# Kernel tuning notes

Measured on AMD Instinct MI355X. Metric: run time of the kernel, lower is better.

Reference implementation:

```python
import jax, jax.numpy as jnp
import numpy as np

D_EMB_IN = 1024
D_K = 64
D_EMB_OUT = 1024
NB_HEADS = 16


def setup_inputs() -> dict:
    key = jax.random.key(0)
    k1, k2, k3, k4, k5 = jax.random.split(key, 5)
    scale = 0.02
    X = jax.random.normal(k1, (2, 2048, D_EMB_IN), dtype=jnp.float32)
    # nn.Linear weights are [out, in]; we store them transposed-ready as [in, out]
    Wq = jax.random.normal(k2, (D_EMB_IN, NB_HEADS * D_K), dtype=jnp.float32) * scale
    Wk = jax.random.normal(k3, (D_EMB_IN, NB_HEADS * D_K), dtype=jnp.float32) * scale
    Wv = jax.random.normal(k4, (D_EMB_IN, NB_HEADS * D_K), dtype=jnp.float32) * scale
    Wo = jax.random.normal(k5, (NB_HEADS * D_K, D_EMB_OUT), dtype=jnp.float32) * scale
    return {"X": X, "Wq": Wq, "Wk": Wk, "Wv": Wv, "Wo": Wo}


def reference(X, Wq, Wk, Wv, Wo):
    B, T, _ = X.shape
    H, Dk = NB_HEADS, D_K
    # project and split heads: [B, H, T, Dk]
    def proj(W):
        return (X @ W).reshape(B, T, H, Dk).transpose(0, 2, 1, 3)
    Q, K, V = proj(Wq), proj(Wk), proj(Wv)
    S = jnp.einsum("bhqd,bhkd->bhqk", Q, K) / jnp.sqrt(jnp.float32(Dk))
    causal = jnp.tril(jnp.ones((T, T), dtype=bool))  # True = keep
    S = jnp.where(causal, S, -jnp.inf)
    P = jax.nn.softmax(S, axis=-1)
    A = jnp.einsum("bhqk,bhkd->bhqd", P, V)
    A = A.transpose(0, 2, 1, 3).reshape(B, T, H * Dk)
    return A @ Wo
```

## Files before the change

### kernel.cpp

```cpp
#include <hip/hip_runtime.h>
#include <hip/hip_bf16.h>


typedef unsigned short u16;
typedef __bf16 bf16x8 __attribute__((ext_vector_type(8)));
typedef float f32x4 __attribute__((ext_vector_type(4)));
typedef u16 u16x4 __attribute__((ext_vector_type(4)));

#define TS 72
#define PS 136
#define NEG_INF (-1e30f)
#define SC_LOG2 0.1803368801f

#if __has_builtin(__builtin_amdgcn_exp2f)
#define EXP2(x) __builtin_amdgcn_exp2f(x)
#else
#define EXP2(x) exp2f(x)
#endif

#define GLD_LDS16(gp, lp) __builtin_amdgcn_global_load_lds( \
    (const __attribute__((address_space(1))) void*)(gp),    \
    (__attribute__((address_space(3))) void*)(lp), 16, 0, 0)

__device__ __forceinline__ bf16x8 as_bf16x8(int4 v) { return __builtin_bit_cast(bf16x8, v); }
__device__ __forceinline__ u16 bf16_bits(float f) { return __builtin_bit_cast(u16, (__bf16)f); }

__device__ __forceinline__ bool detect_f32(const void* X) {
    const u16* x16 = (const u16*)X;
    int lane = threadIdx.x & 63;
    int hits = 0;
#pragma unroll
    for (int i = 0; i < 4; ++i) {
        u16 v = x16[lane * 4 + i];
        hits += (((v >> 7) & 0xFF) > 130) ? 1 : 0;
    }
    return __popcll(__ballot(hits > 0)) >= 8;
}

__device__ __forceinline__ bf16x8 load8(const void* p, size_t eoff, bool f32m) {
    if (!f32m) return as_bf16x8(*(const int4*)((const u16*)p + eoff));
    const float* f = (const float*)p + eoff;
    float4 a = *(const float4*)f;
    float4 b = *(const float4*)(f + 4);
    bf16x8 r;
    r[0] = (__bf16)a.x; r[1] = (__bf16)a.y; r[2] = (__bf16)a.z; r[3] = (__bf16)a.w;
    r[4] = (__bf16)b.x; r[5] = (__bf16)b.y; r[6] = (__bf16)b.z; r[7] = (__bf16)b.w;
    return r;
}

__global__ __launch_bounds__(256) void prep_all(const void* __restrict__ Wq,
                                                const void* __restrict__ Wk,
                                                const void* __restrict__ Wv,
                                                const void* __restrict__ Wo,
                                                const void* __restrict__ X,
                                                u16* __restrict__ Wt3,
                                                u16* __restrict__ Wot,
                                                u16* __restrict__ Xbf) {
    bool f32m = detect_f32(X);
    int z = blockIdx.z;
    if (z == 4) {
        int blk = blockIdx.y * 16 + blockIdx.x;
        size_t base = (size_t)blk * 16384 + threadIdx.x * 8;
#pragma unroll
        for (int i = 0; i < 8; ++i) {
            size_t eoff = base + (size_t)i * 2048;
            bf16x8 v = load8(X, eoff, f32m);
            *(int4*)(Xbf + eoff) = __builtin_bit_cast(int4, v);
        }
        return;
    }
    const void* in = (z == 0) ? Wq : (z == 1) ? Wk : (z == 2) ? Wv : Wo;
    u16* out = (z < 3) ? (Wt3 + (size_t)z * (1u << 20)) : Wot;
    __shared__ alignas(16) u16 T[64][TS];
    int r0 = blockIdx.y * 64, c0 = blockIdx.x * 64;
    int tr = threadIdx.x >> 3, tc8 = threadIdx.x & 7;
    bf16x8 v0 = load8(in, (size_t)(r0 + tr) * 1024 + c0 + tc8 * 8, f32m);
    bf16x8 v1 = load8(in, (size_t)(r0 + tr + 32) * 1024 + c0 + tc8 * 8, f32m);
    *(int4*)&T[tr][tc8 * 8]      = __builtin_bit_cast(int4, v0);
    *(int4*)&T[tr + 32][tc8 * 8] = __builtin_bit_cast(int4, v1);
    __syncthreads();
    for (int half = 0; half < 2; ++half) {
        int cr = tr + half * 32;
        u16 tmp[8];
#pragma unroll
        for (int i = 0; i < 8; ++i) tmp[i] = T[tc8 * 8 + i][cr];
        *(int4*)(out + (size_t)(c0 + cr) * 1024 + r0 + tc8 * 8) = *(int4*)tmp;
    }
}

__global__ __launch_bounds__(256, 4) void gemm128(const u16* __restrict__ A,
                                                  const u16* __restrict__ Bt,
                                                  u16* __restrict__ Cq, u16* __restrict__ Ck,
                                                  u16* __restrict__ Cv) {
    __shared__ alignas(16) u16 As[128 * 64];
    __shared__ alignas(16) u16 Bs[128 * 64];
    const int K = 1024;
    int tid = threadIdx.x, wave = tid >> 6, lane = tid & 63;
    int quad = lane >> 4, l16 = lane & 15;
    int wrow = wave >> 1, wcol = wave & 1;
    int m0 = blockIdx.x * 128, n0 = blockIdx.y * 128;
    int rlane = lane >> 3, kc = lane & 7;
    int scol = (kc ^ rlane) * 8;

    f32x4 acc[4][4] = {};

    for (int k0 = 0; k0 < K; k0 += 64) {
        __syncthreads();
#pragma unroll
        for (int i = 0; i < 4; ++i) {
            int rc = wave * 4 + i;
            GLD_LDS16(A  + (size_t)(m0 + rc * 8 + rlane) * K + k0 + scol, As + rc * 512);
            GLD_LDS16(Bt + (size_t)(n0 + rc * 8 + rlane) * K + k0 + scol, Bs + rc * 512);
        }
        __syncthreads();
#pragma unroll
        for (int ks = 0; ks < 2; ++ks) {
            bf16x8 af[4], bfr[4];
#pragma unroll
            for (int i = 0; i < 4; ++i) {
                int row = wrow * 64 + i * 16 + l16;
                af[i] = as_bf16x8(*(const int4*)(As + row * 64 + (((ks * 4 + quad) ^ (row & 7)) * 8)));
            }
#pragma unroll
            for (int j = 0; j < 4; ++j) {
                int row = wcol * 64 + j * 16 + l16;
                bfr[j] = as_bf16x8(*(const int4*)(Bs + row * 64 + (((ks * 4 + quad) ^ (row & 7)) * 8)));
            }
#pragma unroll
            for (int i = 0; i < 4; ++i)
#pragma unroll
                for (int j = 0; j < 4; ++j)
                    acc[i][j] = __builtin_amdgcn_mfma_f32_16x16x32_bf16(af[i], bfr[j], acc[i][j], 0, 0, 0);
        }
    }

#pragma unroll
    for (int i = 0; i < 4; ++i)
#pragma unroll
        for (int j = 0; j < 4; ++j)
#pragma unroll
            for (int r = 0; r < 4; ++r) {
                int m = m0 + wrow * 64 + i * 16 + quad * 4 + r;
                int n = n0 + wcol * 64 + j * 16 + l16;
                float f = acc[i][j][r];
                if (n < 1024)       Cq[(size_t)m * 1024 + n] = bf16_bits(f);
                else if (n < 2048)  Ck[(size_t)m * 1024 + n - 1024] = bf16_bits(f);
                else {
                    int n2 = n - 2048;
                    int bh = ((m >> 11) << 4) | (n2 >> 6), d = n2 & 63, t = m & 2047;
                    Cv[(((size_t)bh * 64 + d) << 11) + t] = bf16_bits(f);
                }
            }
}

__global__ __launch_bounds__(256, 4) void gemm_out(const u16* __restrict__ A,
                                                   const u16* __restrict__ Bt,
                                                   void* __restrict__ Cout,
                                                   const void* __restrict__ Xdet) {
    bool f32m = detect_f32(Xdet);
    __shared__ alignas(16) u16 As[64 * 128];
    __shared__ alignas(16) u16 Bs[128 * 128];
    const int K = 1024;
    int tid = threadIdx.x, wave = tid >> 6, lane = tid & 63;
    int quad = lane >> 4, l16 = lane & 15;
    int wrow = wave & 1, wcol = wave >> 1;
    int m0 = blockIdx.x * 64, n0 = blockIdx.y * 128;
    int rlane4 = lane >> 4, kc16 = lane & 15;

    f32x4 acc[2][4] = {};

    for (int k0 = 0; k0 < K; k0 += 128) {
        __syncthreads();
#pragma unroll
        for (int i = 0; i < 8; ++i) {
            int rb = wave * 32 + i * 4;
            int grow = rb + rlane4;
            int gch = kc16 ^ (grow & 15);
            GLD_LDS16(Bt + (size_t)(n0 + grow) * K + k0 + gch * 8, Bs + rb * 128);
        }
#pragma unroll
        for (int i = 0; i < 4; ++i) {
            int rb = wave * 16 + i * 4;
            int grow = rb + rlane4;
            int gch = kc16 ^ (grow & 15);
            GLD_LDS16(A + (size_t)(m0 + grow) * K + k0 + gch * 8, As + rb * 128);
        }
        __syncthreads();
#pragma unroll
        for (int ks = 0; ks < 4; ++ks) {
            bf16x8 af[2], bfr[4];
#pragma unroll
            for (int i = 0; i < 2; ++i) {
                int row = wrow * 32 + i * 16 + l16;
                af[i] = as_bf16x8(*(const int4*)(As + row * 128 + (((ks * 4 + quad) ^ (row & 15)) * 8)));
            }
#pragma unroll
            for (int j = 0; j < 4; ++j) {
                int row = wcol * 64 + j * 16 + l16;
                bfr[j] = as_bf16x8(*(const int4*)(Bs + row * 128 + (((ks * 4 + quad) ^ (row & 15)) * 8)));
            }
#pragma unroll
            for (int i = 0; i < 2; ++i)
#pragma unroll
                for (int j = 0; j < 4; ++j)
                    acc[i][j] = __builtin_amdgcn_mfma_f32_16x16x32_bf16(af[i], bfr[j], acc[i][j], 0, 0, 0);
        }
    }

#pragma unroll
    for (int i = 0; i < 2; ++i)
#pragma unroll
        for (int j = 0; j < 4; ++j)
#pragma unroll
            for (int r = 0; r < 4; ++r) {
                int m = m0 + wrow * 32 + i * 16 + quad * 4 + r;
                int n = n0 + wcol * 64 + j * 16 + l16;
                float f = acc[i][j][r];
                if (f32m) ((float*)Cout)[(size_t)m * 1024 + n] = f;
                else      ((u16*)Cout)[(size_t)m * 1024 + n] = bf16_bits(f);
            }
}

__global__ __launch_bounds__(512, 4) void attn_kernel(const u16* __restrict__ Qb,
                                                      const u16* __restrict__ Kb,
                                                      const u16* __restrict__ Vt,
                                                      u16* __restrict__ Ab) {
    __shared__ alignas(16) u16 Ks[128 * 64];
    __shared__ alignas(16) u16 Vs[64 * 128];
    __shared__ alignas(16) u16 Ps[128 * PS];

    int tid = threadIdx.x, wave = tid >> 6, lane = tid & 63;
    int quad = lane >> 4, l16 = lane & 15;
    int bh = blockIdx.x;
    int J = (blockIdx.y < 8) ? (15 - (int)blockIdx.y) : ((int)blockIdx.y - 8);
    int b = bh >> 4, h = bh & 15;
    int q0 = J * 128;
    int kr4 = lane >> 3, kc = lane & 7;
    int vr4 = lane >> 4, vc = lane & 15;

    const u16* qrow = Qb + (size_t)(b * 2048 + q0 + wave * 16 + l16) * 1024 + h * 64;
    bf16x8 qa0 = as_bf16x8(*(const int4*)(qrow + quad * 8));
    bf16x8 qa1 = as_bf16x8(*(const int4*)(qrow + 32 + quad * 8));

    f32x4 o[4] = {};
    float psum = 0.0f;

    const u16* kbase = Kb + (size_t)(b * 2048) * 1024 + h * 64;
    const u16* vbase = Vt + (size_t)bh * 64 * 2048;

    for (int j2 = 0; j2 <= J; ++j2) {
        int t0 = j2 * 128;
        __syncthreads();
#pragma unroll
        for (int i = 0; i < 2; ++i) {
            int rb = (wave * 2 + i) * 8;
            int grow = rb + kr4;
            int gch = kc ^ (grow & 7);
            GLD_LDS16(kbase + (size_t)(t0 + grow) * 1024 + gch * 8, Ks + rb * 64);
        }
#pragma unroll
        for (int i = 0; i < 2; ++i) {
            int rb = (wave * 2 + i) * 4;
            int grow = rb + vr4;
            int gch = vc ^ (grow & 15);
            GLD_LDS16(vbase + (size_t)grow * 2048 + t0 + gch * 8, Vs + rb * 128);
        }
        __syncthreads();

        bool diag = (j2 == J);
        int ntc = diag ? ((wave & ~1) + 2) : 8;

        f32x4 s[8];
        __builtin_amdgcn_s_setprio(1);
#pragma unroll
        for (int nt = 0; nt < 8; ++nt) {
            if (nt >= ntc) continue;
            if (diag && nt > wave) {
                s[nt][0] = NEG_INF; s[nt][1] = NEG_INF; s[nt][2] = NEG_INF; s[nt][3] = NEG_INF;
                continue;
            }
            int row = nt * 16 + l16;
            int sw = row & 7;
            f32x4 a = {};
            bf16x8 b0 = as_bf16x8(*(const int4*)(Ks + row * 64 + ((quad ^ sw) * 8)));
            a = __builtin_amdgcn_mfma_f32_16x16x32_bf16(b0, qa0, a, 0, 0, 0);
            bf16x8 b1 = as_bf16x8(*(const int4*)(Ks + row * 64 + (((4 + quad) ^ sw) * 8)));
            a = __builtin_amdgcn_mfma_f32_16x16x32_bf16(b1, qa1, a, 0, 0, 0);
            a = a * SC_LOG2;
            if (diag && nt == wave) {
#pragma unroll
                for (int r = 0; r < 4; ++r)
                    if (quad * 4 + r > l16) a[r] = NEG_INF;
            }
            s[nt] = a;
        }
        __builtin_amdgcn_s_setprio(0);

        int prow = (wave * 16 + l16) * PS;
#pragma unroll
        for (int nt = 0; nt < 8; ++nt) {
            if (nt >= ntc) continue;
            u16x4 pk;
            float ps4 = 0.0f;
#pragma unroll
            for (int r = 0; r < 4; ++r) {
                float p = EXP2(s[nt][r]);
                ps4 += p;
                pk[r] = bf16_bits(p);
            }
            psum += ps4;
            *(u16x4*)(Ps + prow + nt * 16 + quad * 4) = pk;
        }

        int ksm = ntc >> 1;
        __builtin_amdgcn_s_setprio(1);
#pragma unroll
        for (int ks = 0; ks < 4; ++ks) {
            if (ks >= ksm) continue;
            bf16x8 pa = as_bf16x8(*(const int4*)(Ps + (wave * 16 + l16) * PS + ks * 32 + quad * 8));
#pragma unroll
            for (int d4 = 0; d4 < 4; ++d4) {
                int vrow = d4 * 16 + l16;
                bf16x8 vb = as_bf16x8(*(const int4*)(Vs + vrow * 128 + (((ks * 4 + quad) ^ l16) * 8)));
                o[d4] = __builtin_amdgcn_mfma_f32_16x16x32_bf16(pa, vb, o[d4], 0, 0, 0);
            }
        }
        __builtin_amdgcn_s_setprio(0);
    }

    psum += __shfl_xor(psum, 16);
    psum += __shfl_xor(psum, 32);

    u16* arow = Ab + (size_t)(b * 2048 + q0 + wave * 16) * 1024 + h * 64;
#pragma unroll
    for (int r = 0; r < 4; ++r) {
        float dn = __shfl(psum, quad * 4 + r, 16);
        float inv = 1.0f / dn;
#pragma unroll
        for (int d4 = 0; d4 < 4; ++d4)
            arow[(quad * 4 + r) * 1024 + d4 * 16 + l16] = bf16_bits(o[d4][r] * inv);
    }
}

extern "C" void kernel_launch(void* const* d_in, const int* in_sizes, int n_in,
                              void* d_out, int out_size, void* d_ws, size_t ws_size,
                              hipStream_t stream) {
    (void)in_sizes; (void)n_in; (void)out_size; (void)ws_size;
    const void* X  = d_in[0];
    const void* Wq = d_in[1];
    const void* Wk = d_in[2];
    const void* Wv = d_in[3];
    const void* Wo = d_in[4];
    u16* ws16 = (u16*)d_ws;
    const size_t M1 = 1u << 20;
    u16* Xbf = ws16 + 0 * M1;
    u16* Wt3 = ws16 + 4 * M1;
    u16* Qb  = ws16 + 7 * M1;
    u16* Kb  = ws16 + 11 * M1;
    u16* Vt  = ws16 + 15 * M1;
    u16* Wot = ws16 + 19 * M1;
    u16* Ab  = ws16 + 0 * M1;

    prep_all<<<dim3(16, 16, 5), 256, 0, stream>>>(Wq, Wk, Wv, Wo, X, Wt3, Wot, Xbf);
    gemm128<<<dim3(32, 24), 256, 0, stream>>>(Xbf, Wt3, Qb, Kb, Vt);
    attn_kernel<<<dim3(32, 16), 512, 0, stream>>>(Qb, Kb, Vt, Ab);
    gemm_out<<<dim3(64, 8), 256, 0, stream>>>(Ab, Wot, d_out, X);
}
```

Before: 168.3 us.

## Prefetch next K/V tile into registers to overlap global loads with compute

```diff
diff --git a/kernel.cpp b/kernel.cpp
--- a/kernel.cpp
+++ b/kernel.cpp
@@ -248,25 +248,33 @@
     const u16* kbase = Kb + (size_t)(b * 2048) * 1024 + h * 64;
     const u16* vbase = Vt + (size_t)bh * 64 * 2048;
 
+    int rbk0 = (wave * 2 + 0) * 8, rbk1 = (wave * 2 + 1) * 8;
+    int rbv0 = (wave * 2 + 0) * 4, rbv1 = (wave * 2 + 1) * 4;
+    const u16* kgp0 = kbase + (size_t)(rbk0 + kr4) * 1024 + (kc ^ ((rbk0 + kr4) & 7)) * 8;
+    const u16* kgp1 = kbase + (size_t)(rbk1 + kr4) * 1024 + (kc ^ ((rbk1 + kr4) & 7)) * 8;
+    const u16* vgp0 = vbase + (size_t)(rbv0 + vr4) * 2048 + (vc ^ ((rbv0 + vr4) & 15)) * 8;
+    const u16* vgp1 = vbase + (size_t)(rbv1 + vr4) * 2048 + (vc ^ ((rbv1 + vr4) & 15)) * 8;
+    u16* klp0 = Ks + rbk0 * 64 + lane * 8;
+    u16* klp1 = Ks + rbk1 * 64 + lane * 8;
+    u16* vlp0 = Vs + rbv0 * 128 + lane * 8;
+    u16* vlp1 = Vs + rbv1 * 128 + lane * 8;
+
+    int4 kr0, kr1, vv0, vv1;
+    kr0 = *(const int4*)(kgp0);
+    kr1 = *(const int4*)(kgp1);
+    vv0 = *(const int4*)(vgp0);
+    vv1 = *(const int4*)(vgp1);
+    *(int4*)klp0 = kr0; *(int4*)klp1 = kr1;
+    *(int4*)vlp0 = vv0; *(int4*)vlp1 = vv1;
+    if (J >= 1) {
+        kr0 = *(const int4*)(kgp0 + (size_t)128 * 1024);
+        kr1 = *(const int4*)(kgp1 + (size_t)128 * 1024);
+        vv0 = *(const int4*)(vgp0 + 128);
+        vv1 = *(const int4*)(vgp1 + 128);
+    }
+    __syncthreads();
+
     for (int j2 = 0; j2 <= J; ++j2) {
-        int t0 = j2 * 128;
-        __syncthreads();
-#pragma unroll
-        for (int i = 0; i < 2; ++i) {
-            int rb = (wave * 2 + i) * 8;
-            int grow = rb + kr4;
-            int gch = kc ^ (grow & 7);
-            GLD_LDS16(kbase + (size_t)(t0 + grow) * 1024 + gch * 8, Ks + rb * 64);
-        }
-#pragma unroll
-        for (int i = 0; i < 2; ++i) {
-            int rb = (wave * 2 + i) * 4;
-            int grow = rb + vr4;
-            int gch = vc ^ (grow & 15);
-            GLD_LDS16(vbase + (size_t)grow * 2048 + t0 + gch * 8, Vs + rb * 128);
-        }
-        __syncthreads();
-
         bool diag = (j2 == J);
         int ntc = diag ? ((wave & ~1) + 2) : 8;
 
@@ -326,6 +334,20 @@
             }
         }
         __builtin_amdgcn_s_setprio(0);
+
+        if (j2 < J) {
+            __syncthreads();
+            *(int4*)klp0 = kr0; *(int4*)klp1 = kr1;
+            *(int4*)vlp0 = vv0; *(int4*)vlp1 = vv1;
+            if (j2 + 2 <= J) {
+                size_t t0n = (size_t)(j2 + 2) * 128;
+                kr0 = *(const int4*)(kgp0 + t0n * 1024);
+                kr1 = *(const int4*)(kgp1 + t0n * 1024);
+                vv0 = *(const int4*)(vgp0 + t0n);
+                vv1 = *(const int4*)(vgp1 + t0n);
+            }
+            __syncthreads();
+        }
     }
 
     psum += __shfl_xor(psum, 16);
```

Measured after the change: 179.1 us. +6.4%, slower.

## Double-buffer K/V tiles in attention and interleave softmax with PV per chunk

Applied to the files above, without the earlier changes.

```diff
diff --git a/kernel.cpp b/kernel.cpp
--- a/kernel.cpp
+++ b/kernel.cpp
@@ -8,7 +8,7 @@
 typedef u16 u16x4 __attribute__((ext_vector_type(4)));
 
 #define TS 72
-#define PS 136
+#define PSQ 40
 #define NEG_INF (-1e30f)
 #define SC_LOG2 0.1803368801f
 
@@ -221,13 +221,95 @@
             }
 }
 
+
+#define STAGE_TILE(KSBUF, VSBUF, T0)                                           \
+    {                                                                          \
+        _Pragma("unroll")                                                      \
+        for (int i_ = 0; i_ < 2; ++i_) {                                       \
+            int rb_ = (wave * 2 + i_) * 8;                                     \
+            int grow_ = rb_ + kr4;                                             \
+            int gch_ = kc ^ (grow_ & 7);                                       \
+            GLD_LDS16(kbase + (size_t)((T0) + grow_) * 1024 + gch_ * 8,        \
+                      KSBUF + rb_ * 64);                                       \
+        }                                                                      \
+        _Pragma("unroll")                                                      \
+        for (int i_ = 0; i_ < 2; ++i_) {                                       \
+            int rb_ = (wave * 2 + i_) * 4;                                     \
+            int grow_ = rb_ + vr4;                                             \
+            int gch_ = vc ^ (grow_ & 15);                                      \
+            GLD_LDS16(vbase + (size_t)grow_ * 2048 + (T0) + gch_ * 8,          \
+                      VSBUF + rb_ * 128);                                      \
+        }                                                                      \
+    }
+
+#define COMPUTE_TILE(KS, VS, DIAG, NTC)                                        \
+    {                                                                          \
+        _Pragma("unroll")                                                      \
+        for (int g = 0; g < 4; ++g) {                                          \
+            if (2 * g >= (NTC)) continue;                                      \
+            f32x4 sg0, sg1;                                                    \
+            __builtin_amdgcn_s_setprio(1);                                     \
+            _Pragma("unroll")                                                  \
+            for (int h2 = 0; h2 < 2; ++h2) {                                   \
+                int nt = 2 * g + h2;                                           \
+                f32x4 a = {};                                                  \
+                if ((DIAG) && nt > wave) {                                     \
+                    a[0] = NEG_INF; a[1] = NEG_INF;                            \
+                    a[2] = NEG_INF; a[3] = NEG_INF;                            \
+                } else {                                                       \
+                    int row = nt * 16 + l16;                                   \
+                    int sw = row & 7;                                          \
+                    bf16x8 b0 = as_bf16x8(*(const int4*)((KS) + row * 64 + ((quad ^ sw) * 8)));       \
+                    a = __builtin_amdgcn_mfma_f32_16x16x32_bf16(b0, qa0, a, 0, 0, 0);                 \
+                    bf16x8 b1 = as_bf16x8(*(const int4*)((KS) + row * 64 + (((4 + quad) ^ sw) * 8))); \
+                    a = __builtin_amdgcn_mfma_f32_16x16x32_bf16(b1, qa1, a, 0, 0, 0);                 \
+                    a = a * SC_LOG2;                                           \
+                    if ((DIAG) && nt == wave) {                                \
+                        _Pragma("unroll")                                      \
+                        for (int r = 0; r < 4; ++r)                            \
+                            if (quad * 4 + r > l16) a[r] = NEG_INF;            \
+                    }                                                          \
+                }                                                              \
+                if (h2 == 0) sg0 = a; else sg1 = a;                            \
+            }                                                                  \
+            __builtin_amdgcn_s_setprio(0);                                     \
+            _Pragma("unroll")                                                  \
+            for (int h2 = 0; h2 < 2; ++h2) {                                   \
+                f32x4 sv = h2 ? sg1 : sg0;                                     \
+                u16x4 pk;                                                      \
+                float ps4 = 0.0f;                                              \
+                _Pragma("unroll")                                              \
+                for (int r = 0; r < 4; ++r) {                                  \
+                    float p = EXP2(sv[r]);                                     \
+                    ps4 += p;                                                  \
+                    pk[r] = bf16_bits(p);                                      \
+                }                                                              \
+                psum += ps4;                                                   \
+                *(u16x4*)(Ps + prow + h2 * 16 + quad * 4) = pk;                \
+            }                                                                  \
+            __builtin_amdgcn_s_setprio(1);                                     \
+            {                                                                  \
+                bf16x8 pa = as_bf16x8(*(const int4*)(Ps + prow + quad * 8));   \
+                _Pragma("unroll")                                              \
+                for (int d4 = 0; d4 < 4; ++d4) {                               \
+                    int vrow = d4 * 16 + l16;                                  \
+                    bf16x8 vb = as_bf16x8(*(const int4*)((VS) + vrow * 128 + (((g * 4 + quad) ^ l16) * 8))); \
+                    o[d4] = __builtin_amdgcn_mfma_f32_16x16x32_bf16(pa, vb, o[d4], 0, 0, 0);          \
+                }                                                              \
+            }                                                                  \
+            __builtin_amdgcn_s_setprio(0);                                     \
+        }                                                                      \
+    }
+
 __global__ __launch_bounds__(512, 4) void attn_kernel(const u16* __restrict__ Qb,
                                                       const u16* __restrict__ Kb,
                                                       const u16* __restrict__ Vt,
                                                       u16* __restrict__ Ab) {
-    __shared__ alignas(16) u16 Ks[128 * 64];
-    __shared__ alignas(16) u16 Vs[64 * 128];
-    __shared__ alignas(16) u16 Ps[128 * PS];
+    __shared__ alignas(16) u16 Ks0[128 * 64];
+    __shared__ alignas(16) u16 Ks1[128 * 64];
+    __shared__ alignas(16) u16 Vs0[64 * 128];
+    __shared__ alignas(16) u16 Vs1[64 * 128];
+    __shared__ alignas(16) u16 Ps[128 * PSQ];
 
     int tid = threadIdx.x, wave = tid >> 6, lane = tid & 63;
     int quad = lane >> 4, l16 = lane & 15;
@@ -244,88 +326,30 @@
 
     f32x4 o[4] = {};
     float psum = 0.0f;
+    int prow = (wave * 16 + l16) * PSQ;
 
     const u16* kbase = Kb + (size_t)(b * 2048) * 1024 + h * 64;
     const u16* vbase = Vt + (size_t)bh * 64 * 2048;
 
-    for (int j2 = 0; j2 <= J; ++j2) {
-        int t0 = j2 * 128;
-        __syncthreads();
-#pragma unroll
-        for (int i = 0; i < 2; ++i) {
-            int rb = (wave * 2 + i) * 8;
-            int grow = rb + kr4;
-            int gch = kc ^ (grow & 7);
-            GLD_LDS16(kbase + (size_t)(t0 + grow) * 1024 + gch * 8, Ks + rb * 64);
-        }
-#pragma unroll
-        for (int i = 0; i < 2; ++i) {
-            int rb = (wave * 2 + i) * 4;
-            int grow = rb + vr4;
-            int gch = vc ^ (grow & 15);
-            GLD_LDS16(vbase + (size_t)grow * 2048 + t0 + gch * 8, Vs + rb * 128);
-        }
-        __syncthreads();
-
-        bool diag = (j2 == J);
-        int ntc = diag ? ((wave & ~1) + 2) : 8;
-
-        f32x4 s[8];
-        __builtin_amdgcn_s_setprio(1);
-#pragma unroll
-        for (int nt = 0; nt < 8; ++nt) {
-            if (nt >= ntc) continue;
-            if (diag && nt > wave) {
-                s[nt][0] = NEG_INF; s[nt][1] = NEG_INF; s[nt][2] = NEG_INF; s[nt][3] = NEG_INF;
-                continue;
-            }
-            int row = nt * 16 + l16;
-            int sw = row & 7;
-            f32x4 a = {};
-            bf16x8 b0 = as_bf16x8(*(const int4*)(Ks + row * 64 + ((quad ^ sw) * 8)));
-            a = __builtin_amdgcn_mfma_f32_16x16x32_bf16(b0, qa0, a, 0, 0, 0);
-            bf16x8 b1 = as_bf16x8(*(const int4*)(Ks + row * 64 + (((4 + quad) ^ sw) * 8)));
-            a = __builtin_amdgcn_mfma_f32_16x16x32_bf16(b1, qa1, a, 0, 0, 0);
-            a = a * SC_LOG2;
-            if (diag && nt == wave) {
-#pragma unroll
-                for (int r = 0; r < 4; ++r)
-                    if (quad * 4 + r > l16) a[r] = NEG_INF;
-            }
-            s[nt] = a;
-        }
-        __builtin_amdgcn_s_setprio(0);
-
-        int prow = (wave * 16 + l16) * PS;
-#pragma unroll
-        for (int nt = 0; nt < 8; ++nt) {
-            if (nt >= ntc) continue;
-            u16x4 pk;
-            float ps4 = 0.0f;
-#pragma unroll
-            for (int r = 0; r < 4; ++r) {
-                float p = EXP2(s[nt][r]);
-                ps4 += p;
-                pk[r] = bf16_bits(p);
-            }
-            psum += ps4;
-            *(u16x4*)(Ps + prow + nt * 16 + quad * 4) = pk;
-        }
-
-        int ksm = ntc >> 1;
-        __builtin_amdgcn_s_setprio(1);
-#pragma unroll
-        for (int ks = 0; ks < 4; ++ks) {
-            if (ks >= ksm) continue;
-            bf16x8 pa = as_bf16x8(*(const int4*)(Ps + (wave * 16 + l16) * PS + ks * 32 + quad * 8));
-#pragma unroll
-            for (int d4 = 0; d4 < 4; ++d4) {
-                int vrow = d4 * 16 + l16;
-                bf16x8 vb = as_bf16x8(*(const int4*)(Vs + vrow * 128 + (((ks * 4 + quad) ^ l16) * 8)));
-                o[d4] = __builtin_amdgcn_mfma_f32_16x16x32_bf16(pa, vb, o[d4], 0, 0, 0);
-            }
-        }
-        __builtin_amdgcn_s_setprio(0);
+    STAGE_TILE(Ks0, Vs0, 0);
+    __syncthreads();
+
+    for (int j2 = 0; j2 <= J; j2 += 2) {
+        if (j2 + 1 <= J) STAGE_TILE(Ks1, Vs1, (j2 + 1) * 128);
+        {
+            bool diag = (j2 == J);
+            int ntc = diag ? ((wave & ~1) + 2) : 8;
+            COMPUTE_TILE(Ks0, Vs0, diag, ntc);
+        }
+        __syncthreads();
+        if (j2 + 1 > J) break;
+        if (j2 + 2 <= J) STAGE_TILE(Ks0, Vs0, (j2 + 2) * 128);
+        {
+            bool diag = (j2 + 1 == J);
+            int ntc = diag ? ((wave & ~1) + 2) : 8;
+            COMPUTE_TILE(Ks1, Vs1, diag, ntc);
+        }
+        __syncthreads();
     }
 
     psum += __shfl_xor(psum, 16);
```

New measurement: 173.0 us. 2.8% more time.

## Keep attention P in registers via lane shuffles; swizzle GEMM block order

Applied to the files above, without the earlier changes.

```diff
diff --git a/kernel.cpp b/kernel.cpp
--- a/kernel.cpp
+++ b/kernel.cpp
@@ -5,10 +5,8 @@
 typedef unsigned short u16;
 typedef __bf16 bf16x8 __attribute__((ext_vector_type(8)));
 typedef float f32x4 __attribute__((ext_vector_type(4)));
-typedef u16 u16x4 __attribute__((ext_vector_type(4)));
 
 #define TS 72
-#define PS 136
 #define NEG_INF (-1e30f)
 #define SC_LOG2 0.1803368801f
 
@@ -98,7 +96,10 @@
     int tid = threadIdx.x, wave = tid >> 6, lane = tid & 63;
     int quad = lane >> 4, l16 = lane & 15;
     int wrow = wave >> 1, wcol = wave & 1;
-    int m0 = blockIdx.x * 128, n0 = blockIdx.y * 128;
+    int flat = (int)(blockIdx.x + gridDim.x * blockIdx.y);
+    int logical = (flat & 7) * 96 + (flat >> 3);
+    int m0 = (logical & 31) * 128;
+    int n0 = (logical >> 5) * 128;
     int rlane = lane >> 3, kc = lane & 7;
     int scol = (kc ^ rlane) * 8;
 
@@ -227,7 +228,6 @@
                                                       u16* __restrict__ Ab) {
     __shared__ alignas(16) u16 Ks[128 * 64];
     __shared__ alignas(16) u16 Vs[64 * 128];
-    __shared__ alignas(16) u16 Ps[128 * PS];
 
     int tid = threadIdx.x, wave = tid >> 6, lane = tid & 63;
     int quad = lane >> 4, l16 = lane & 15;
@@ -247,6 +247,10 @@
 
     const u16* kbase = Kb + (size_t)(b * 2048) * 1024 + h * 64;
     const u16* vbase = Vt + (size_t)bh * 64 * 2048;
+
+    int qb0 = quad & 1, qb1 = quad >> 1;
+    int src1 = (qb0 << 5) | (qb1 << 4) | l16;
+    int src2 = (qb0 << 5) | ((1 - qb1) << 4) | l16;
 
     for (int j2 = 0; j2 <= J; ++j2) {
         int t0 = j2 * 128;
@@ -296,20 +300,15 @@
         }
         __builtin_amdgcn_s_setprio(0);
 
-        int prow = (wave * 16 + l16) * PS;
+        unsigned pk[8][2];
 #pragma unroll
         for (int nt = 0; nt < 8; ++nt) {
             if (nt >= ntc) continue;
-            u16x4 pk;
-            float ps4 = 0.0f;
-#pragma unroll
-            for (int r = 0; r < 4; ++r) {
-                float p = EXP2(s[nt][r]);
-                ps4 += p;
-                pk[r] = bf16_bits(p);
-            }
-            psum += ps4;
-            *(u16x4*)(Ps + prow + nt * 16 + quad * 4) = pk;
+            float p0 = EXP2(s[nt][0]), p1 = EXP2(s[nt][1]);
+            float p2 = EXP2(s[nt][2]), p3 = EXP2(s[nt][3]);
+            psum += (p0 + p1) + (p2 + p3);
+            pk[nt][0] = (unsigned)bf16_bits(p0) | ((unsigned)bf16_bits(p1) << 16);
+            pk[nt][1] = (unsigned)bf16_bits(p2) | ((unsigned)bf16_bits(p3) << 16);
         }
 
         int ksm = ntc >> 1;
@@ -317,7 +316,20 @@
 #pragma unroll
         for (int ks = 0; ks < 4; ++ks) {
             if (ks >= ksm) continue;
-            bf16x8 pa = as_bf16x8(*(const int4*)(Ps + (wave * 16 + l16) * PS + ks * 32 + quad * 8));
+            int v10 = qb0 ? (int)pk[2 * ks + 1][0] : (int)pk[2 * ks][0];
+            int v11 = qb0 ? (int)pk[2 * ks + 1][1] : (int)pk[2 * ks][1];
+            int v20 = qb0 ? (int)pk[2 * ks][0] : (int)pk[2 * ks + 1][0];
+            int v21 = qb0 ? (int)pk[2 * ks][1] : (int)pk[2 * ks + 1][1];
+            int r10 = __shfl(v10, src1, 64);
+            int r11 = __shfl(v11, src1, 64);
+            int r20 = __shfl(v20, src2, 64);
+            int r21 = __shfl(v21, src2, 64);
+            int4 paw;
+            paw.x = qb1 ? r20 : r10;
+            paw.y = qb1 ? r21 : r11;
+            paw.z = qb1 ? r10 : r20;
+            paw.w = qb1 ? r11 : r21;
+            bf16x8 pa = as_bf16x8(paw);
 #pragma unroll
             for (int d4 = 0; d4 < 4; ++d4) {
                 int vrow = d4 * 16 + l16;
```

Result: slower. 184.2 us (+9.4%).
